# Performance work log

Hardware: AMD Instinct MI355X
Metric: run time of the kernel (lower is better)

## Reference

```python
import jax, jax.numpy as jnp
import numpy as np

LMAX = 2
NC = (LMAX + 1) ** 2          # 9 spherical-harmonic coefficients
C = 128                       # sphere/hidden channels (scalar_dim = 256//2)
CIN = 256                     # input/output irrep channels
EC = 16                       # edge channels (attn_weight_input_dim//2)
N_ATOM = 512
TOPK = 8
E = N_ATOM * TOPK
RES = 18                      # SO3 grid resolution

# m-primary permutation from CoefficientMapping(lmax=2, mmax=2).to_m:
# m=0 real [0,2,6]; m=1 real [3,7]; m=1 imag [1,5]; m=2 real [8]; m=2 imag [4]
PERM = np.array([0, 2, 6, 3, 7, 1, 5, 8, 4])
INV_PERM = np.argsort(PERM)
DEG = np.array([0, 1, 1, 1, 2, 2, 2, 2, 2])  # degree l of each coefficient


def _so2_block(em, x_edge, d0w, d0b, m0w1, m0w2,
               m1dw, m1db, m1w1r, m1w2r, m1w1i, m1w2i,
               m2dw, m2db, m2w1r, m2w2r, m2w1i, m2w2i):
    # em: [E, 9, C] (l-primary); x_edge: [E, EC]
    En = em.shape[0]
    em = em[:, PERM]                                  # -> m-primary order
    # m = 0 block (3 coefficients)
    g0 = jax.nn.silu(x_edge @ d0w + d0b)              # [E, C]
    x0 = em[:, 0:3].reshape(En, 3 * C)
    x0 = (((x0 @ m0w1) * g0) @ m0w2).reshape(En, 3, C)

    def so2_conv(xm, dw, db, w1r, w2r, w1i, w2i):
        # xm: [E, 2, k*C] with (real, imag) stacked on axis 1
        ge = jax.nn.silu(x_edge @ dw + db).reshape(En, 2, C)
        xr = jnp.einsum('eti,ih->eth', xm, w1r) * ge[:, 0:1]
        xr = jnp.einsum('eth,ho->eto', xr, w2r)
        xi = jnp.einsum('eti,ih->eth', xm, w1i) * ge[:, 1:2]
        xi = jnp.einsum('eth,ho->eto', xi, w2i)
        return jnp.stack([xr[:, 0] - xi[:, 1], xr[:, 1] + xi[:, 0]], axis=1)

    x1 = so2_conv(em[:, 3:7].reshape(En, 2, 2 * C), m1dw, m1db, m1w1r, m1w2r, m1w1i, m1w2i).reshape(En, 4, C)
    x2 = so2_conv(em[:, 7:9].reshape(En, 2, C), m2dw, m2db, m2w1r, m2w2r, m2w1i, m2w2i).reshape(En, 2, C)
    em = jnp.concatenate([x0, x1, x2], axis=1)
    return em[:, INV_PERM]                            # back to l-primary


def _forward(x, attn_weight, wigner, to_grid, from_grid, w_in, b_in, w_out, b_out,
             emb_src, emb_tgt, fc_dist_w, fc_dist_b, fc_edge_w, fc_edge_b,
             so2_dist0_w, so2_dist0_b, so2_m0_w1, so2_m0_w2,
             so2_m1_dist_w, so2_m1_dist_b, so2_m1_w1r, so2_m1_w2r, so2_m1_w1i, so2_m1_w2i,
             so2_m2_dist_w, so2_m2_dist_b, so2_m2_w1r, so2_m2_w2r, so2_m2_w1i, so2_m2_w2i,
             atomic_numbers, edge_src, attn_mask):
    N, topK = attn_weight.shape[:2]
    Eg = N * topK
    # proj_input: per-degree SO3 linear 256 -> 128, bias on l=0 only
    h = jnp.einsum('nic,ico->nio', x, w_in[DEG])
    h = h.at[:, 0, :].add(b_in)
    edge_tgt = jnp.repeat(jnp.arange(N), topK)
    # edge feature: dist MLP + source/target atom-type embedding gathers
    xe = attn_weight.reshape(Eg, -1) @ fc_dist_w + fc_dist_b
    xe = xe + emb_src[atomic_numbers][edge_src] + emb_tgt[atomic_numbers][edge_tgt]
    xe = jax.nn.silu(jax.nn.silu(xe) @ fc_edge_w + fc_edge_b)
    # gather node features to edges + rotate into edge frame (Wigner D)
    xs = jnp.einsum('eij,ejc->eic', wigner, h[edge_src])
    xt = jnp.einsum('eij,ejc->eic', wigner, h[edge_tgt])

    def blk(b, em):
        return _so2_block(em, xe, so2_dist0_w[b], so2_dist0_b[b], so2_m0_w1[b], so2_m0_w2[b],
                          so2_m1_dist_w[b], so2_m1_dist_b[b], so2_m1_w1r[b], so2_m1_w2r[b], so2_m1_w1i[b], so2_m1_w2i[b],
                          so2_m2_dist_w[b], so2_m2_dist_b[b], so2_m2_w1r[b], so2_m2_w2r[b], so2_m2_w1i[b], so2_m2_w2i[b])

    xt = blk(0, xs) + blk(1, xt)
    # grid activation: to-grid, SiLU, from-grid
    xg = jax.nn.silu(jnp.einsum('bai,eic->ebac', to_grid, xt))
    xt = jnp.einsum('bai,ebac->eic', from_grid, xg)
    # inverse rotation (orthogonal Wigner -> transpose)
    xt = jnp.einsum('eji,ejc->eic', wigner, xt)
    # mask invalid neighbors, scatter-sum over topK
    out = xt.reshape(N, topK, NC, C)
    out = jnp.where(attn_mask[:, :, None, None], 0.0, out).sum(axis=1)
    # proj_final: per-degree SO3 linear 128 -> 256
    out = jnp.einsum('nic,ico->nio', out, w_out[DEG])
    return out.at[:, 0, :].add(b_out)


def setup_inputs() -> dict:
    key = jax.random.key(0)
    ks = jax.random.split(key, 40)
    s = 0.05
    inp = {
        'x': jax.random.normal(ks[0], (N_ATOM, NC, CIN), jnp.float32),
        'attn_weight': jax.random.normal(ks[1], (N_ATOM, TOPK, 32), jnp.float32),
        'wigner': jax.random.normal(ks[2], (E, NC, NC), jnp.float32) * 0.3,
        'to_grid': jax.random.normal(ks[3], (RES, RES, NC), jnp.float32) * 0.2,
        'from_grid': jax.random.normal(ks[4], (RES, RES, NC), jnp.float32) * 0.2,
        'w_in': jax.random.normal(ks[5], (3, CIN, C), jnp.float32) * s,
        'b_in': jax.random.normal(ks[6], (C,), jnp.float32) * s,
        'w_out': jax.random.normal(ks[7], (3, C, CIN), jnp.float32) * s,
        'b_out': jax.random.normal(ks[8], (CIN,), jnp.float32) * s,
        'emb_src': jax.random.uniform(ks[9], (256, EC), jnp.float32, -0.001, 0.001),
        'emb_tgt': jax.random.uniform(ks[10], (256, EC), jnp.float32, -0.001, 0.001),
        'fc_dist_w': jax.random.normal(ks[11], (32, EC), jnp.float32) * s,
        'fc_dist_b': jax.random.normal(ks[12], (EC,), jnp.float32) * s,
        'fc_edge_w': jax.random.normal(ks[13], (EC, EC), jnp.float32) * s,
        'fc_edge_b': jax.random.normal(ks[14], (EC,), jnp.float32) * s,
        'so2_dist0_w': jax.random.normal(ks[15], (2, EC, C), jnp.float32) * s,
        'so2_dist0_b': jax.random.normal(ks[16], (2, C), jnp.float32) * s,
        'so2_m0_w1': jax.random.normal(ks[17], (2, 3 * C, C), jnp.float32) * s,
        'so2_m0_w2': jax.random.normal(ks[18], (2, C, 3 * C), jnp.float32) * s,
        'so2_m1_dist_w': jax.random.normal(ks[19], (2, EC, 2 * C), jnp.float32) * s,
        'so2_m1_dist_b': jax.random.normal(ks[20], (2, 2 * C), jnp.float32) * s,
        'so2_m1_w1r': jax.random.normal(ks[21], (2, 2 * C, C), jnp.float32) * s,
        'so2_m1_w2r': jax.random.normal(ks[22], (2, C, 2 * C), jnp.float32) * s,
        'so2_m1_w1i': jax.random.normal(ks[23], (2, 2 * C, C), jnp.float32) * s,
        'so2_m1_w2i': jax.random.normal(ks[24], (2, C, 2 * C), jnp.float32) * s,
        'so2_m2_dist_w': jax.random.normal(ks[25], (2, EC, 2 * C), jnp.float32) * s,
        'so2_m2_dist_b': jax.random.normal(ks[26], (2, 2 * C), jnp.float32) * s,
        'so2_m2_w1r': jax.random.normal(ks[27], (2, C, C), jnp.float32) * s,
        'so2_m2_w2r': jax.random.normal(ks[28], (2, C, C), jnp.float32) * s,
        'so2_m2_w1i': jax.random.normal(ks[29], (2, C, C), jnp.float32) * s,
        'so2_m2_w2i': jax.random.normal(ks[30], (2, C, C), jnp.float32) * s,
        'atomic_numbers': jax.random.randint(ks[31], (N_ATOM,), 0, 256),
        'edge_src': jax.random.randint(ks[32], (E,), 0, N_ATOM),
        'attn_mask': jax.random.randint(ks[33], (N_ATOM, TOPK), 0, 2).astype(bool),
    }
    return inp


def reference(x, attn_weight, wigner, to_grid, from_grid, w_in, b_in, w_out, b_out,
              emb_src, emb_tgt, fc_dist_w, fc_dist_b, fc_edge_w, fc_edge_b,
              so2_dist0_w, so2_dist0_b, so2_m0_w1, so2_m0_w2,
              so2_m1_dist_w, so2_m1_dist_b, so2_m1_w1r, so2_m1_w2r, so2_m1_w1i, so2_m1_w2i,
              so2_m2_dist_w, so2_m2_dist_b, so2_m2_w1r, so2_m2_w2r, so2_m2_w1i, so2_m2_w2i,
              atomic_numbers, edge_src, attn_mask):
    return _forward(x, attn_weight, wigner, to_grid, from_grid, w_in, b_in, w_out, b_out,
                    emb_src, emb_tgt, fc_dist_w, fc_dist_b, fc_edge_w, fc_edge_b,
                    so2_dist0_w, so2_dist0_b, so2_m0_w1, so2_m0_w2,
                    so2_m1_dist_w, so2_m1_dist_b, so2_m1_w1r, so2_m1_w2r, so2_m1_w1i, so2_m1_w2i,
                    so2_m2_dist_w, so2_m2_dist_b, so2_m2_w1r, so2_m2_w2r, so2_m2_w1i, so2_m2_w2i,
                    atomic_numbers, edge_src, attn_mask)
```

## Files before the change

### kernel.cpp

```cpp
#include <hip/hip_runtime.h>
#include <math.h>

typedef __attribute__((ext_vector_type(8))) short short8;
typedef __attribute__((ext_vector_type(4))) float f32x4;

__device__ const int d_PERM[9] = {0,2,6,3,7,1,5,8,4};
__device__ const int d_DEG[9]  = {0,1,1,1,2,2,2,2,2};

__device__ __forceinline__ float silu_f(float x){ return x / (1.0f + __expf(-x)); }

__device__ __forceinline__ unsigned short f2bf(float f){
  unsigned int u = __float_as_uint(f);
  return (unsigned short)((u + 0x7FFFu + ((u >> 16) & 1u)) >> 16);
}

__device__ __forceinline__ int mask_at(const void* mp, int flag, int e){
  if (flag==1) return ((const unsigned char*)mp)[e] != 0;
  if (flag==3) return ((const unsigned int*)mp)[2*e] != 0u;
  return ((const unsigned int*)mp)[e] != 0u;
}

__global__ void k_detect(const unsigned int* __restrict__ w, int* __restrict__ flag){
  __shared__ int notI, notF, anyOdd, anyEven;
  if (threadIdx.x==0){ notI=0; notF=0; anyOdd=0; anyEven=0; }
  __syncthreads();
  int li=0, lf=0, lo=0, le=0;
  for (int i = threadIdx.x; i < 1024; i += 256){
    unsigned int v = w[i];
    if (v != 0u && v != 1u) li = 1;
    if (v != 0u && v != 0x3F800000u) lf = 1;
    if (v != 0u){ if (i & 1) lo = 1; else le = 1; }
  }
  if (li) atomicOr(&notI,1);
  if (lf) atomicOr(&notF,1);
  if (lo) atomicOr(&anyOdd,1);
  if (le) atomicOr(&anyEven,1);
  __syncthreads();
  if (threadIdx.x==0){
    int f;
    if (!notI) f = (anyOdd || !anyEven) ? 0 : 3;
    else       f = (!notF) ? 2 : 1;
    *flag = f;
  }
}

__global__ __launch_bounds__(256) void k_compact(const void* __restrict__ maskp,
    const int* __restrict__ flagp, int* __restrict__ list, int* __restrict__ count){
  __shared__ int cnt[256];
  __shared__ int offs[256];
  int f = *flagp;
  int tid = threadIdx.x;
  int base = tid*16;
  int c = 0;
  for (int i=0;i<16;i++) if (!mask_at(maskp, f, base+i)) c++;
  cnt[tid] = c;
  __syncthreads();
  if (tid==0){
    int r = 0;
    for (int i=0;i<256;i++){ offs[i] = r; r += cnt[i]; }
    *count = r;
  }
  __syncthreads();
  int w = offs[tid];
  for (int i=0;i<16;i++){
    int e = base+i;
    if (!mask_at(maskp, f, e)) list[w++] = e;
  }
}

__global__ __launch_bounds__(128) void k_h(const float* __restrict__ x,
    const float* __restrict__ w_in, const float* __restrict__ b_in,
    float* __restrict__ H){
  __shared__ float xl[16][260];
  int i = blockIdx.y; int n0 = blockIdx.x*16;
  int deg = d_DEG[i];
  for (int idx = threadIdx.x; idx < 16*256; idx += 128){
    int r = idx >> 8, c = idx & 255;
    xl[r][c] = x[((size_t)(n0+r)*9 + i)*256 + c];
  }
  __syncthreads();
  int o = threadIdx.x;
  float acc[16];
  #pragma unroll
  for (int r=0;r<16;r++) acc[r]=0.f;
  const float* w = w_in + (size_t)deg*32768 + o;
  for (int c=0;c<256;c+=4){
    float w0=w[(size_t)c*128], w1=w[(size_t)(c+1)*128], w2=w[(size_t)(c+2)*128], w3=w[(size_t)(c+3)*128];
    #pragma unroll
    for (int r=0;r<16;r++){
      float4 xv4 = *(const float4*)&xl[r][c];
      acc[r] += xv4.x*w0 + xv4.y*w1 + xv4.z*w2 + xv4.w*w3;
    }
  }
  float bb = (i==0)? b_in[o] : 0.f;
  #pragma unroll
  for (int r=0;r<16;r++) H[((size_t)(n0+r)*9+i)*128+o] = acc[r]+bb;
}

__global__ __launch_bounds__(256) void k_xe(const float* __restrict__ attn,
    const float* __restrict__ fdw, const float* __restrict__ fdb,
    const float* __restrict__ few, const float* __restrict__ feb,
    const float* __restrict__ es, const float* __restrict__ et,
    const int* __restrict__ an, const int* __restrict__ esrc,
    float* __restrict__ XE){
  int e = blockIdx.x*256 + threadIdx.x;
  float aw[32];
  #pragma unroll
  for (int k=0;k<32;k+=4){
    float4 v = *(const float4*)&attn[(size_t)e*32+k];
    aw[k]=v.x; aw[k+1]=v.y; aw[k+2]=v.z; aw[k+3]=v.w;
  }
  int src = esrc[e]; int tgt = e>>3;
  int za = an[src], zb = an[tgt];
  float v0[16];
  #pragma unroll
  for (int j=0;j<16;j++){
    float s = fdb[j] + es[(size_t)za*16+j] + et[(size_t)zb*16+j];
    #pragma unroll
    for (int k=0;k<32;k++) s += aw[k]*fdw[k*16+j];
    v0[j] = silu_f(s);
  }
  #pragma unroll
  for (int j=0;j<16;j++){
    float s = feb[j];
    #pragma unroll
    for (int k=0;k<16;k++) s += v0[k]*few[k*16+j];
    XE[(size_t)e*16+j] = silu_f(s);
  }
}

__global__ __launch_bounds__(256) void k_wcvt(
    const float* __restrict__ m0w1, const float* __restrict__ m1w1r, const float* __restrict__ m1w1i,
    const float* __restrict__ m2w1r, const float* __restrict__ m2w1i,
    const float* __restrict__ m0w2, const float* __restrict__ m1w2r, const float* __restrict__ m1w2i,
    const float* __restrict__ m2w2r, const float* __restrict__ m2w2i,
    unsigned short* __restrict__ Wt)
{
  int base = (blockIdx.x*256 + threadIdx.x)*4;
  #pragma unroll
  for (int ii = 0; ii < 4; ii++){
    int idx = base + ii;
    float v;
    if (idx < 98304){
      int p = idx/49152, r = idx%49152, n = r/384, k = r%384;
      v = m0w1[p*49152 + k*128 + n];
    } else if (idx < 229376){
      int j = idx-98304; int q = j/32768, r = j%32768, n = r/256, k = r%256;
      const float* w = (q&1)?m1w1i:m1w1r;
      v = w[(q>>1)*32768 + k*128 + n];
    } else if (idx < 294912){
      int j = idx-229376; int q = j/16384, r = j%16384, n = r/128, k = r%128;
      const float* w = (q&1)?m2w1i:m2w1r;
      v = w[(q>>1)*16384 + k*128 + n];
    } else if (idx < 393216){
      int j = idx-294912; int n = j/256, k = j%256;
      v = m0w2[(k>>7)*49152 + (k&127)*384 + n];
    } else if (idx < 524288){
      int j = idx-393216; int n = j/512, k = j%512;
      const float* w = ((k>>7)&1)?m1w2i:m1w2r;
      v = w[(k>>8)*32768 + (k&127)*256 + n];
    } else {
      int j = idx-524288; int n = j/512, k = j%512;
      const float* w = ((k>>7)&1)?m2w2i:m2w2r;
      v = w[(k>>8)*16384 + (k&127)*128 + n];
    }
    Wt[idx] = f2bf(v);
  }
}

__global__ __launch_bounds__(256) void k_rotgate_m(
    const float* __restrict__ Hg, const float* __restrict__ XEg,
    const int* __restrict__ esrc, const float* __restrict__ wig,
    const float* __restrict__ d0w,  const float* __restrict__ d0b,
    const float* __restrict__ m1dw, const float* __restrict__ m1db,
    const float* __restrict__ m2dw, const float* __restrict__ m2db,
    unsigned short* __restrict__ XSb, unsigned short* __restrict__ XTb,
    float* __restrict__ G,
    const int* __restrict__ list, const int* __restrict__ countp, int s0)
{
  int slot = s0 + blockIdx.x;
  if (slot >= *countp) return;
  __shared__ float xe16[16];
  int e = list[slot];
  int el = blockIdx.x;
  int tid = threadIdx.x;
  int n = e >> 3, src = esrc[e];
  if (tid < 16) xe16[tid] = XEg[(size_t)e*16 + tid];
  for (int idx = tid; idx < 1152; idx += 256){
    int p = idx >> 7, c = idx & 127;
    int ch = d_PERM[p];
    const float* wr = wig + (size_t)e*81 + ch*9;
    const float* hs = Hg + (size_t)src*1152 + c;
    const float* ht = Hg + (size_t)n*1152 + c;
    float s1 = 0.f, s2 = 0.f;
    #pragma unroll
    for (int j = 0; j < 9; j++){
      float wv = wr[j];
      s1 += wv * hs[j*128];
      s2 += wv * ht[j*128];
    }
    XSb[(size_t)el*1152 + idx] = f2bf(s1);
    XTb[(size_t)el*1152 + idx] = f2bf(s2);
  }
  __syncthreads();
  for (int col = tid; col < 1280; col += 256){
    int b = col / 640, r = col % 640;
    const float* w; float bias; int ldw, c2;
    if (r < 128){       w = d0w  + (size_t)b*2048; c2 = r;     ldw = 128; bias = d0b[b*128 + c2]; }
    else if (r < 384){  w = m1dw + (size_t)b*4096; c2 = r-128; ldw = 256; bias = m1db[b*256 + c2]; }
    else {              w = m2dw + (size_t)b*4096; c2 = r-384; ldw = 256; bias = m2db[b*256 + c2]; }
    float s = bias;
    #pragma unroll
    for (int kk = 0; kk < 16; kk++) s += xe16[kk] * w[kk*ldw + c2];
    G[(size_t)el*1280 + col] = silu_f(s);
  }
}

__global__ __launch_bounds__(256) void k_gs1m(
    const unsigned short* __restrict__ XSb, const unsigned short* __restrict__ XTb,
    const float* __restrict__ G, const unsigned short* __restrict__ Wt,
    unsigned short* __restrict__ Pgb,
    const int* __restrict__ countp, int s0)
{
  int lc = *countp - s0;
  if (lc <= 0) return;
  if (lc > 2048) lc = 2048;
  int b = blockIdx.x, t = threadIdx.x;
  const unsigned short* Ax; const unsigned short* Bw;
  int K, bm, obase, goff, rsh, aoff, tstride;
  if (b < 64){
    int path = b & 1, mt = b >> 1;
    Ax = path ? XTb : XSb;
    Bw = Wt + path*49152;
    K = 384; bm = mt*64; obase = path*128; goff = path ? 640 : 0;
    rsh = 0; aoff = 0; tstride = 0;
  } else if (b < 320){
    int i = b-64; int q = i>>6, mt = i&63;
    Ax = (q>=2) ? XTb : XSb;
    Bw = Wt + 98304 + q*32768;
    K = 256; bm = mt*64; obase = 256 + q*256; goff = 128 + (q&1)*128 + (q>>1)*640;
    rsh = 1; aoff = 384; tstride = 256;
  } else {
    int i = b-320; int q = i>>6, mt = i&63;
    Ax = (q>=2) ? XTb : XSb;
    Bw = Wt + 229376 + q*16384;
    K = 128; bm = mt*64; obase = 1280 + q*256; goff = 384 + (q&1)*128 + (q>>1)*640;
    rsh = 1; aoff = 896; tstride = 128;
  }
  int rows = rsh ? 2*lc : lc;
  if (bm >= rows) return;
  int w = t >> 6, l = t & 63;
  int am = bm + w*16 + (l & 15);
  int ael = am >> rsh, atp = am & rsh;
  const unsigned short* aptr = Ax + (size_t)ael*1152 + aoff + atp*tstride + ((l>>4)*8);
  int bn = l & 15;
  int bko = (l>>4)*8;
  f32x4 acc[8];
  #pragma unroll
  for (int i=0;i<8;i++){ acc[i][0]=0.f; acc[i][1]=0.f; acc[i][2]=0.f; acc[i][3]=0.f; }
  for (int k0 = 0; k0 < K; k0 += 32){
    short8 a = *(const short8*)(aptr + k0);
    #pragma unroll
    for (int nt = 0; nt < 8; nt++){
      const unsigned short* bp = Bw + (size_t)(nt*16 + bn)*K + k0 + bko;
      short8 bb = *(const short8*)bp;
      acc[nt] = __builtin_amdgcn_mfma_f32_16x16x32_bf16(a, bb, acc[nt], 0, 0, 0);
    }
  }
  #pragma unroll
  for (int nt = 0; nt < 8; nt++){
    #pragma unroll
    for (int r = 0; r < 4; r++){
      int i2 = (l>>4)*4 + r;
      int m = bm + w*16 + i2;
      int el = m >> rsh, tp = m & rsh;
      int h = nt*16 + (l & 15);
      float v = acc[nt][r] * G[(size_t)el*1280 + goff + h];
      Pgb[(size_t)el*2304 + obase + tp*128 + h] = f2bf(v);
    }
  }
}

__global__ __launch_bounds__(256) void k_gs2m(
    const unsigned short* __restrict__ Pgb, const unsigned short* __restrict__ Wt2,
    float* __restrict__ Y,
    const int* __restrict__ countp, int s0)
{
  int lc = *countp - s0;
  if (lc <= 0) return;
  if (lc > 2048) lc = 2048;
  int b = blockIdx.x, t = threadIdx.x;
  int region, bm, ncb, K, rsh, segb;
  const unsigned short* Bw;
  if (b < 96){ region=0; int mt=b/3, nt3=b-mt*3; bm=mt*64; ncb=nt3*128; K=256; rsh=0; segb=0;    Bw = Wt2; }
  else if (b < 224){ region=1; int i=b-96; int mt=i>>1, nt2=i&1; bm=mt*64; ncb=nt2*128; K=512; rsh=1; segb=256;  Bw = Wt2 + 98304; }
  else { region=2; int mt=b-224; bm=mt*64; ncb=0; K=512; rsh=1; segb=1280; Bw = Wt2 + 229376; }
  int rows = rsh ? 2*lc : lc;
  if (bm >= rows) return;
  int w = t >> 6, l = t & 63;
  int am = bm + w*16 + (l & 15);
  int ael = am >> rsh, atp = am & rsh;
  int bko = (l>>4)*8;
  f32x4 acc[8];
  #pragma unroll
  for (int i=0;i<8;i++){ acc[i][0]=0.f; acc[i][1]=0.f; acc[i][2]=0.f; acc[i][3]=0.f; }
  for (int k0 = 0; k0 < K; k0 += 32){
    const unsigned short* ap;
    short sm = 0;
    if (region == 0){
      ap = Pgb + (size_t)ael*2304 + k0 + bko;
    } else {
      int seg = k0 >> 7, kk = k0 & 127;
      int tsel = (seg&1) ? (1-atp) : atp;
      sm = (short)(((seg&1) && atp==0) ? 0x8000 : 0);
      ap = Pgb + (size_t)ael*2304 + segb + seg*256 + tsel*128 + kk + bko;
    }
    short8 a = *(const short8*)ap;
    short8 smv = (short8)sm;
    a ^= smv;
    #pragma unroll
    for (int nt = 0; nt < 8; nt++){
      const unsigned short* bp = Bw + (size_t)(ncb + nt*16 + (l&15))*K + k0 + bko;
      short8 bb = *(const short8*)bp;
      acc[nt] = __builtin_amdgcn_mfma_f32_16x16x32_bf16(a, bb, acc[nt], 0, 0, 0);
    }
  }
  #pragma unroll
  for (int nt = 0; nt < 8; nt++){
    #pragma unroll
    for (int r = 0; r < 4; r++){
      int i2 = (l>>4)*4 + r;
      int m = bm + w*16 + i2;
      int el = m >> rsh, tp = m & rsh;
      int col = ncb + nt*16 + (l&15);
      int g = col >> 7, c = col & 127;
      int ch;
      if (region==0)      ch = (g==0) ? 0 : ((g==1) ? 2 : 6);
      else if (region==1) ch = tp ? (g ? 5 : 1) : (g ? 7 : 3);
      else                ch = tp ? 4 : 8;
      Y[(size_t)(s0 + el)*1152 + ch*128 + c] = acc[nt][r];
    }
  }
}

__global__ __launch_bounds__(256, 8) void k_grid9(const float* __restrict__ Y,
    const float* __restrict__ wig, const float* __restrict__ tg, const float* __restrict__ fg,
    const int* __restrict__ list, const int* __restrict__ countp,
    float* __restrict__ R)
{
  const int cnt = *countp;
  const int epair = blockIdx.x >> 1;
  const int half  = blockIdx.x & 1;
  const int base = epair*2;
  if (base >= cnt) return;
  __shared__ float cf[162*24];
  __shared__ float wl[2*81];
  int tid = threadIdx.x;
  int ok1 = (base+1 < cnt);
  int s2[2], e2[2];
  s2[0] = base;
  s2[1] = ok1 ? base+1 : base;
  e2[0] = list[s2[0]];
  e2[1] = list[s2[1]];

  const float* tgh = tg + half*1458;
  const float* fgh = fg + half*1458;
  for (int idx = tid; idx < 1458; idx += 256){
    int p = idx / 9, i = idx - p*9;
    cf[p*24 + i]      = tgh[idx];
    cf[p*24 + 12 + i] = fgh[idx];
  }
  for (int i = tid; i < 162; i += 256){
    int eL2 = i / 81, ii = i - eL2*81;
    wl[i] = wig[(size_t)e2[eL2]*81 + ii];
  }
  __syncthreads();

  int eL = tid >> 7, c = tid & 127;
  if (eL == 1 && !ok1) return;
  int slot = s2[eL], e = e2[eL];

  float y[9], z[9];
  #pragma unroll
  for (int i = 0; i < 9; i++){
    y[i] = Y[(size_t)slot*1152 + i*128 + c];
    z[i] = 0.f;
  }

  #pragma unroll 2
  for (int p = 0; p < 162; p++){
    const float* cp = &cf[p*24];
    float4 t0 = *(const float4*)cp;
    float4 t1 = *(const float4*)(cp+4);
    float  t8 = cp[8];
    float gp = t0.x*y[0] + t0.y*y[1] + t0.z*y[2] + t0.w*y[3]
             + t1.x*y[4] + t1.y*y[5] + t1.z*y[6] + t1.w*y[7] + t8*y[8];
    float s = gp * __fdividef(1.0f, 1.0f + __expf(-gp));
    float4 f0 = *(const float4*)(cp+12);
    float4 f1 = *(const float4*)(cp+16);
    float  f8 = cp[20];
    z[0] += f0.x*s; z[1] += f0.y*s; z[2] += f0.z*s; z[3] += f0.w*s;
    z[4] += f1.x*s; z[5] += f1.y*s; z[6] += f1.z*s; z[7] += f1.w*s; z[8] += f8*s;
  }

  const float* wle = &wl[eL*81];
  #pragma unroll
  for (int i2 = 0; i2 < 9; i2++){
    float s = 0.f;
    #pragma unroll
    for (int j = 0; j < 9; j++) s += wle[j*9 + i2] * z[j];
    atomicAdd(&R[(size_t)e*1152 + i2*128 + c], s);
  }
}

__global__ __launch_bounds__(256) void k_redout2(const float* __restrict__ R,
    const void* __restrict__ maskp, const int* __restrict__ flagp,
    const float* __restrict__ w_out, const float* __restrict__ b_out,
    float* __restrict__ out){
  __shared__ float sacc[128];
  int i2 = blockIdx.x; int n = blockIdx.y;
  int tid = threadIdx.x;
  int f = *flagp;
  if (tid < 128){
    float a = 0.f;
    for (int k = 0; k < 8; k++){
      int e = n*8 + k;
      if (!mask_at(maskp, f, e)) a += R[(size_t)e*1152 + i2*128 + tid];
    }
    sacc[tid] = a;
  }
  __syncthreads();
  int o = tid;
  int deg = d_DEG[i2];
  const float* wp = w_out + (size_t)deg*32768 + o;
  float s = (i2==0) ? b_out[o] : 0.f;
  #pragma unroll 4
  for (int c = 0; c < 128; c += 4){
    float4 a = *(const float4*)&sacc[c];
    s += a.x*wp[(size_t)c*256] + a.y*wp[(size_t)(c+1)*256]
       + a.z*wp[(size_t)(c+2)*256] + a.w*wp[(size_t)(c+3)*256];
  }
  out[((size_t)n*9 + i2)*256 + o] = s;
}

__device__ __forceinline__ float dotW(const float* __restrict__ A, const float* __restrict__ Wm, int K){
  float s = 0.f;
  #pragma unroll 4
  for (int i=0;i<K;i+=4){
    float4 a = *(const float4*)&A[i];
    s += a.x*Wm[(size_t)i*128] + a.y*Wm[(size_t)(i+1)*128]
       + a.z*Wm[(size_t)(i+2)*128] + a.w*Wm[(size_t)(i+3)*128];
  }
  return s;
}
__device__ __forceinline__ float dot2W(const float* __restrict__ P0, const float* __restrict__ P1,
    const float* __restrict__ W0, const float* __restrict__ W1, int ldw){
  float s = 0.f;
  #pragma unroll 4
  for (int k=0;k<128;k+=4){
    float4 a = *(const float4*)&P0[k];
    float4 b = *(const float4*)&P1[k];
    s += a.x*W0[(size_t)k*ldw] + a.y*W0[(size_t)(k+1)*ldw] + a.z*W0[(size_t)(k+2)*ldw] + a.w*W0[(size_t)(k+3)*ldw];
    s += b.x*W1[(size_t)k*ldw] + b.y*W1[(size_t)(k+1)*ldw] + b.z*W1[(size_t)(k+2)*ldw] + b.w*W1[(size_t)(k+3)*ldw];
  }
  return s;
}

__global__ __launch_bounds__(256) void k_mega(
    const float* __restrict__ x,      const float* __restrict__ w_in,  const float* __restrict__ b_in,
    const float* __restrict__ attn,
    const float* __restrict__ fdw,    const float* __restrict__ fdb,
    const float* __restrict__ few,    const float* __restrict__ feb,
    const float* __restrict__ es,     const float* __restrict__ et,
    const int*   __restrict__ an,     const int*   __restrict__ esrc,
    const float* __restrict__ d0w,    const float* __restrict__ d0b,
    const float* __restrict__ m1dw,   const float* __restrict__ m1db,
    const float* __restrict__ m2dw,   const float* __restrict__ m2db,
    const float* __restrict__ m0w1,   const float* __restrict__ m0w2,
    const float* __restrict__ m1w1r,  const float* __restrict__ m1w2r,
    const float* __restrict__ m1w1i,  const float* __restrict__ m1w2i,
    const float* __restrict__ m2w1r,  const float* __restrict__ m2w2r,
    const float* __restrict__ m2w1i,  const float* __restrict__ m2w2i,
    const float* __restrict__ wig,    const float* __restrict__ tg,   const float* __restrict__ fg,
    const float* __restrict__ w_out,  const float* __restrict__ b_out,
    const void*  __restrict__ maskp,  const int* __restrict__ flagp,
    float* __restrict__ out)
{
  __shared__ float S[7168];
  float* acc  = S;
  float* xs   = S + 1152;
  float* xtl  = S + 2304;
  float* Zb   = S + 1152;
  float* gg   = S + 3456;
  float* Yb   = S + 3456;
  float* P    = S + 4736;
  float* wl   = S + 7040;
  float* xe16 = S + 7124;
  float* xv   = S + 7140;

  const int n   = blockIdx.x;
  const int tid = threadIdx.x;
  const int f   = *flagp;

  for (int i = tid; i < 1152; i += 256) acc[i] = 0.f;

  for (int k = 0; k < 8; k++){
    int e = n*8 + k;
    if (mask_at(maskp, f, e)) continue;
    int src = esrc[e];
    __syncthreads();
    for (int i = tid; i < 81; i += 256) wl[i] = wig[(size_t)e*81 + i];
    if (tid < 16){
      int j = tid;
      float s = fdb[j] + es[(size_t)an[src]*16 + j] + et[(size_t)an[n]*16 + j];
      for (int kk = 0; kk < 32; kk++) s += attn[(size_t)e*32 + kk] * fdw[kk*16 + j];
      xv[j] = silu_f(s);
    }
    for (int idx = tid; idx < 2304; idx += 256){
      int which = idx >= 1152;
      int lidx = idx - which*1152;
      int j = lidx >> 7, c = lidx & 127;
      int deg = d_DEG[j];
      const float* wp = w_in + (size_t)deg*32768 + c;
      const float* xp = x + ((size_t)(which ? n : src)*9 + j)*256;
      float s = (j==0) ? b_in[c] : 0.f;
      for (int cc = 0; cc < 256; cc++) s += xp[cc] * wp[cc*128];
      P[idx] = s;
    }
    __syncthreads();
    if (tid < 16){
      int j = tid;
      float s = feb[j];
      for (int kk = 0; kk < 16; kk++) s += xv[kk] * few[kk*16 + j];
      xe16[j] = silu_f(s);
    }
    for (int idx = tid; idx < 1152; idx += 256){
      int p = idx >> 7, c = idx & 127;
      int ch = d_PERM[p];
      float s1 = 0.f, s2 = 0.f;
      #pragma unroll
      for (int j = 0; j < 9; j++){
        float wv = wl[ch*9 + j];
        s1 += wv * P[j*128 + c];
        s2 += wv * P[1152 + j*128 + c];
      }
      xs[idx]  = s1;
      xtl[idx] = s2;
    }
    __syncthreads();
    for (int col = tid; col < 1280; col += 256){
      int b = col / 640, r = col % 640;
      const float* w; float bias; int ldw, c2;
      if (r < 128){       w = d0w  + (size_t)b*2048; c2 = r;     ldw = 128; bias = d0b[b*128 + c2]; }
      else if (r < 384){  w = m1dw + (size_t)b*4096; c2 = r-128; ldw = 256; bias = m1db[b*256 + c2]; }
      else {              w = m2dw + (size_t)b*4096; c2 = r-384; ldw = 256; bias = m2db[b*256 + c2]; }
      float s = bias;
      #pragma unroll
      for (int kk = 0; kk < 16; kk++) s += xe16[kk] * w[kk*ldw + c2];
      gg[col] = silu_f(s);
    }
    __syncthreads();
    for (int o = tid; o < 2304; o += 256){
      float s;
      if (o < 256){
        int path = o >> 7, h = o & 127;
        s = dotW(path ? xtl : xs, m0w1 + (size_t)path*49152 + h, 384);
      } else if (o < 1280){
        int q = (o-256) >> 8; int rem = (o-256) & 255; int t = rem >> 7, h = rem & 127;
        const float* A  = ((q>=2) ? xtl : xs) + 384 + t*256;
        const float* Wm = ((q&1) ? m1w1i : m1w1r) + (size_t)((q>=2)?1:0)*32768 + h;
        s = dotW(A, Wm, 256);
      } else {
        int q = (o-1280) >> 8; int rem = (o-1280) & 255; int t = rem >> 7, h = rem & 127;
        const float* A  = ((q>=2) ? xtl : xs) + 896 + t*128;
        const float* Wm = ((q&1) ? m2w1i : m2w1r) + (size_t)((q>=2)?1:0)*16384 + h;
        s = dotW(A, Wm, 128);
      }
      P[o] = s;
    }
    __syncthreads();
    for (int o = tid; o < 2304; o += 256){
      int h = o & 127, goff;
      if (o < 256) goff = (o >> 7) ? 640 : 0;
      else if (o < 1280){ int q = (o-256) >> 8;  goff = 128 + (q&1)*128 + (q>>1)*640; }
      else              { int q = (o-1280) >> 8; goff = 384 + (q&1)*128 + (q>>1)*640; }
      P[o] *= gg[goff + h];
    }
    __syncthreads();
    for (int o = tid; o < 1152; o += 256){
      float s; int ch, c;
      if (o < 384){
        int g = o >> 7; c = o & 127;
        ch = (g==0) ? 0 : ((g==1) ? 2 : 6);
        const float* w0 = m0w2 + o;
        s = dot2W(P, P+128, w0, w0+49152, 384);
      } else if (o < 896){
        int om = o - 384; int tp = om >> 8; int col = om & 255;
        int g = col >> 7; c = col & 127;
        ch = tp ? (g ? 5 : 1) : (g ? 7 : 3);
        float sgn = tp ? 1.f : -1.f;
        const float* wr = m1w2r + col;
        const float* wi = m1w2i + col;
        s = dot2W(P+256+tp*128,     P+768+tp*128,     wr, wr+32768, 256)
          + sgn * dot2W(P+512+(1-tp)*128, P+1024+(1-tp)*128, wi, wi+32768, 256);
      } else {
        int om = o - 896; int tp = om >> 7; c = om & 127;
        ch = tp ? 4 : 8;
        float sgn = tp ? 1.f : -1.f;
        const float* wr = m2w2r + c;
        const float* wi = m2w2i + c;
        s = dot2W(P+1280+tp*128,     P+1792+tp*128,     wr, wr+16384, 128)
          + sgn * dot2W(P+1536+(1-tp)*128, P+2048+(1-tp)*128, wi, wi+16384, 128);
      }
      Yb[ch*128 + c] = s;
    }
    __syncthreads();
    {
      int half = tid >> 7, c = tid & 127;
      float z[9];
      #pragma unroll
      for (int i = 0; i < 9; i++) z[i] = 0.f;
      float y[9];
      #pragma unroll
      for (int i = 0; i < 9; i++) y[i] = Yb[i*128 + c];
      int p0 = half*162, p1 = p0 + 162;
      #pragma unroll 2
      for (int p = p0; p < p1; p++){
        float gp = 0.f;
        #pragma unroll
        for (int i = 0; i < 9; i++) gp += tg[p*9 + i] * y[i];
        float s = silu_f(gp);
        #pragma unroll
        for (int i = 0; i < 9; i++) z[i] += fg[p*9 + i] * s;
      }
      #pragma unroll
      for (int i = 0; i < 9; i++) Zb[half*1152 + i*128 + c] = z[i];
    }
    __syncthreads();
    for (int idx = tid; idx < 1152; idx += 256){
      int i2 = idx >> 7, c = idx & 127;
      float s = 0.f;
      #pragma unroll
      for (int j = 0; j < 9; j++)
        s += wl[j*9 + i2] * (Zb[j*128 + c] + Zb[1152 + j*128 + c]);
      acc[idx] += s;
    }
  }
  __syncthreads();
  {
    int o = tid;
    for (int i2 = 0; i2 < 9; i2++){
      int deg = d_DEG[i2];
      const float* wp = w_out + (size_t)deg*32768 + o;
      float s = (i2==0) ? b_out[o] : 0.f;
      #pragma unroll 4
      for (int c = 0; c < 128; c += 4){
        float4 a = *(const float4*)&acc[i2*128 + c];
        s += a.x*wp[(size_t)c*256] + a.y*wp[(size_t)(c+1)*256]
           + a.z*wp[(size_t)(c+2)*256] + a.w*wp[(size_t)(c+3)*256];
      }
      out[((size_t)n*9 + i2)*256 + o] = s;
    }
  }
}

extern "C" void kernel_launch(void* const* d_in, const int* in_sizes, int n_in,
                              void* d_out, int out_size, void* d_ws, size_t ws_size,
                              hipStream_t stream){
  const float* x     = (const float*)d_in[0];
  const float* attn  = (const float*)d_in[1];
  const float* wig   = (const float*)d_in[2];
  const float* tg    = (const float*)d_in[3];
  const float* fg    = (const float*)d_in[4];
  const float* w_in  = (const float*)d_in[5];
  const float* b_in  = (const float*)d_in[6];
  const float* w_out = (const float*)d_in[7];
  const float* b_out = (const float*)d_in[8];
  const float* es    = (const float*)d_in[9];
  const float* et    = (const float*)d_in[10];
  const float* fdw   = (const float*)d_in[11];
  const float* fdb   = (const float*)d_in[12];
  const float* few   = (const float*)d_in[13];
  const float* feb   = (const float*)d_in[14];
  const float* d0w   = (const float*)d_in[15];
  const float* d0b   = (const float*)d_in[16];
  const float* m0w1  = (const float*)d_in[17];
  const float* m0w2  = (const float*)d_in[18];
  const float* m1dw  = (const float*)d_in[19];
  const float* m1db  = (const float*)d_in[20];
  const float* m1w1r = (const float*)d_in[21];
  const float* m1w2r = (const float*)d_in[22];
  const float* m1w1i = (const float*)d_in[23];
  const float* m1w2i = (const float*)d_in[24];
  const float* m2dw  = (const float*)d_in[25];
  const float* m2db  = (const float*)d_in[26];
  const float* m2w1r = (const float*)d_in[27];
  const float* m2w2r = (const float*)d_in[28];
  const float* m2w1i = (const float*)d_in[29];
  const float* m2w2i = (const float*)d_in[30];
  const int*   an    = (const int*)d_in[31];
  const int*   esrc  = (const int*)d_in[32];
  const void*  maskp = d_in[33];

  int*   ip  = (int*)d_ws;
  int* FLAG  = ip + 0;
  int* COUNT = ip + 1;
  int* LIST  = ip + 16;
  float* W   = (float*)d_ws;
  float* Hg1  = W + 4112;
  float* XEg1 = Hg1 + 589824;
  float* XS1  = XEg1 + 65536;
  float* XT1  = XS1 + 2359296;
  float* Gg1  = XT1 + 2359296;
  float* Pg1  = Gg1 + 2621440;
  float* Yf   = Pg1 + 4718592;
  float* Rf   = XS1;
  unsigned short* XSb = (unsigned short*)XS1;
  unsigned short* XTb = XSb + 2359296;
  unsigned short* Pgb = XSb + 4718592;
  unsigned short* Wtb = (unsigned short*)Pg1;
  size_t need_t1 = (size_t)(4112 + 589824 + 65536 + 2359296 + 2359296 + 2621440 + 4718592 + 4718592) * 4;

  k_detect<<<1,256,0,stream>>>((const unsigned int*)maskp, FLAG);

  if (ws_size >= need_t1){
    k_compact<<<1,256,0,stream>>>(maskp, FLAG, LIST, COUNT);
    k_h<<<dim3(32,9),128,0,stream>>>(x, w_in, b_in, Hg1);
    k_xe<<<16,256,0,stream>>>(attn, fdw, fdb, few, feb, es, et, an, esrc, XEg1);
    k_wcvt<<<576,256,0,stream>>>(m0w1, m1w1r, m1w1i, m2w1r, m2w1i,
                                 m0w2, m1w2r, m1w2i, m2w2r, m2w2i, Wtb);
    for (int c2 = 0; c2 < 2; c2++){
      int s0 = c2*2048;
      k_rotgate_m<<<2048,256,0,stream>>>(Hg1, XEg1, esrc, wig,
          d0w, d0b, m1dw, m1db, m2dw, m2db, XSb, XTb, Gg1, LIST, COUNT, s0);
      k_gs1m<<<576,256,0,stream>>>(XSb, XTb, Gg1, Wtb, Pgb, COUNT, s0);
      k_gs2m<<<288,256,0,stream>>>(Pgb, Wtb + 294912, Yf, COUNT, s0);
    }
    hipMemsetAsync(Rf, 0, (size_t)4718592*4, stream);
    k_grid9<<<4096,256,0,stream>>>(Yf, wig, tg, fg, LIST, COUNT, Rf);
    k_redout2<<<dim3(9,512),256,0,stream>>>(Rf, maskp, FLAG, w_out, b_out, (float*)d_out);
  } else {
    k_mega<<<512,256,0,stream>>>(
        x, w_in, b_in, attn, fdw, fdb, few, feb, es, et, an, esrc,
        d0w, d0b, m1dw, m1db, m2dw, m2db,
        m0w1, m0w2, m1w1r, m1w2r, m1w1i, m1w2i, m2w1r, m2w2r, m2w1i, m2w2i,
        wig, tg, fg, w_out, b_out, maskp, FLAG, (float*)d_out);
  }
}
```

Measured before the change: 315.4 us.

## Compute SO3 grid projection with bf16 MFMA and drop atomic accumulation

Replaces the scalar FP32 grid kernel with an MFMA-based one. It projects coefficients to grid points, applies SiLU, and projects back with 16x16x32 bf16 matrix instructions, using a one-time repacked bf16 copy of the to/from grid matrices. The previous GEMM now writes its output as bf16 in a channel-major padded layout suited to the MFMA operand. Each edge's result is written directly instead of through atomicAdd, which also removes the float memset of R. The cost is bf16 rounding of the activations and grid values, plus a new memset of the padded Y buffer.

```diff
diff --git a/kernel.cpp b/kernel.cpp
--- a/kernel.cpp
+++ b/kernel.cpp
@@ -2,6 +2,7 @@
 #include <math.h>
 
 typedef __attribute__((ext_vector_type(8))) short short8;
+typedef __attribute__((ext_vector_type(4))) short short4_t;
 typedef __attribute__((ext_vector_type(4))) float f32x4;
 
 __device__ const int d_PERM[9] = {0,2,6,3,7,1,5,8,4};
@@ -165,6 +166,26 @@
       v = w[(k>>8)*16384 + (k&127)*128 + n];
     }
     Wt[idx] = f2bf(v);
+  }
+}
+
+__global__ __launch_bounds__(256) void k_fprep(const float* __restrict__ tg,
+    const float* __restrict__ fg,
+    unsigned short* __restrict__ tgA, unsigned short* __restrict__ fgA)
+{
+  for (int idx = threadIdx.x; idx < 11264; idx += 256){
+    int pt = idx >> 9, rem = idx & 511, l = rem >> 3, j = rem & 7;
+    int p = pt*16 + (l & 15);
+    int i = (l >> 4)*8 + j;
+    float v = (p < 324 && i < 9) ? tg[p*9 + i] : 0.f;
+    tgA[idx] = f2bf(v);
+  }
+  for (int idx = threadIdx.x; idx < 5632; idx += 256){
+    int sb = idx >> 9, rem = idx & 511, l = rem >> 3, j = rem & 7;
+    int p = sb*32 + (l >> 4)*8 + j;
+    int i = l & 15;
+    float v = (p < 324 && i < 9) ? fg[p*9 + i] : 0.f;
+    fgA[idx] = f2bf(v);
   }
 }
 
@@ -283,7 +304,7 @@
 
 __global__ __launch_bounds__(256) void k_gs2m(
     const unsigned short* __restrict__ Pgb, const unsigned short* __restrict__ Wt2,
-    float* __restrict__ Y,
+    unsigned short* __restrict__ Ybt,
     const int* __restrict__ countp, int s0)
 {
   int lc = *countp - s0;
@@ -338,78 +359,71 @@
       if (region==0)      ch = (g==0) ? 0 : ((g==1) ? 2 : 6);
       else if (region==1) ch = tp ? (g ? 5 : 1) : (g ? 7 : 3);
       else                ch = tp ? 4 : 8;
-      Y[(size_t)(s0 + el)*1152 + ch*128 + c] = acc[nt][r];
-    }
-  }
-}
-
-__global__ __launch_bounds__(256, 8) void k_grid9(const float* __restrict__ Y,
-    const float* __restrict__ wig, const float* __restrict__ tg, const float* __restrict__ fg,
+      Ybt[(size_t)(s0 + el)*2048 + c*16 + ch] = f2bf(acc[nt][r]);
+    }
+  }
+}
+
+__global__ __launch_bounds__(256) void k_gridm(
+    const unsigned short* __restrict__ Ybt,
+    const unsigned short* __restrict__ tgA, const unsigned short* __restrict__ fgA,
+    const float* __restrict__ wig,
     const int* __restrict__ list, const int* __restrict__ countp,
     float* __restrict__ R)
 {
-  const int cnt = *countp;
-  const int epair = blockIdx.x >> 1;
-  const int half  = blockIdx.x & 1;
-  const int base = epair*2;
-  if (base >= cnt) return;
-  __shared__ float cf[162*24];
-  __shared__ float wl[2*81];
+  int slot = blockIdx.x;
+  if (slot >= *countp) return;
+  __shared__ float wl[81];
+  __shared__ unsigned short Sld[4][512];
+  __shared__ float Zld[4][256];
   int tid = threadIdx.x;
-  int ok1 = (base+1 < cnt);
-  int s2[2], e2[2];
-  s2[0] = base;
-  s2[1] = ok1 ? base+1 : base;
-  e2[0] = list[s2[0]];
-  e2[1] = list[s2[1]];
-
-  const float* tgh = tg + half*1458;
-  const float* fgh = fg + half*1458;
-  for (int idx = tid; idx < 1458; idx += 256){
-    int p = idx / 9, i = idx - p*9;
-    cf[p*24 + i]      = tgh[idx];
-    cf[p*24 + 12 + i] = fgh[idx];
-  }
-  for (int i = tid; i < 162; i += 256){
-    int eL2 = i / 81, ii = i - eL2*81;
-    wl[i] = wig[(size_t)e2[eL2]*81 + ii];
-  }
-  __syncthreads();
-
-  int eL = tid >> 7, c = tid & 127;
-  if (eL == 1 && !ok1) return;
-  int slot = s2[eL], e = e2[eL];
-
-  float y[9], z[9];
-  #pragma unroll
-  for (int i = 0; i < 9; i++){
-    y[i] = Y[(size_t)slot*1152 + i*128 + c];
-    z[i] = 0.f;
-  }
-
-  #pragma unroll 2
-  for (int p = 0; p < 162; p++){
-    const float* cp = &cf[p*24];
-    float4 t0 = *(const float4*)cp;
-    float4 t1 = *(const float4*)(cp+4);
-    float  t8 = cp[8];
-    float gp = t0.x*y[0] + t0.y*y[1] + t0.z*y[2] + t0.w*y[3]
-             + t1.x*y[4] + t1.y*y[5] + t1.z*y[6] + t1.w*y[7] + t8*y[8];
-    float s = gp * __fdividef(1.0f, 1.0f + __expf(-gp));
-    float4 f0 = *(const float4*)(cp+12);
-    float4 f1 = *(const float4*)(cp+16);
-    float  f8 = cp[20];
-    z[0] += f0.x*s; z[1] += f0.y*s; z[2] += f0.z*s; z[3] += f0.w*s;
-    z[4] += f1.x*s; z[5] += f1.y*s; z[6] += f1.z*s; z[7] += f1.w*s; z[8] += f8*s;
-  }
-
-  const float* wle = &wl[eL*81];
-  #pragma unroll
-  for (int i2 = 0; i2 < 9; i2++){
-    float s = 0.f;
-    #pragma unroll
-    for (int j = 0; j < 9; j++) s += wle[j*9 + i2] * z[j];
-    atomicAdd(&R[(size_t)e*1152 + i2*128 + c], s);
+  int e = list[slot];
+  for (int i = tid; i < 81; i += 256) wl[i] = wig[(size_t)e*81 + i];
+  __syncthreads();
+  int w = tid >> 6, l = tid & 63;
+  int lcn = l & 15, lg = l >> 4;
+  const unsigned short* ybase = Ybt + (size_t)slot*2048;
+
+  for (int ct = 0; ct < 2; ct++){
+    int c0 = (w*2 + ct)*16;
+    short8 bfA = (short8)(short)0;
+    if (lg < 2) bfA = *(const short8*)(ybase + (c0 + lcn)*16 + lg*8);
+    f32x4 Z; Z[0]=0.f; Z[1]=0.f; Z[2]=0.f; Z[3]=0.f;
+    for (int sb = 0; sb < 11; sb++){
+      f32x4 s0; s0[0]=0.f; s0[1]=0.f; s0[2]=0.f; s0[3]=0.f;
+      f32x4 s1 = s0;
+      short8 a0 = *(const short8*)(tgA + (size_t)(sb*2+0)*512 + l*8);
+      short8 a1 = *(const short8*)(tgA + (size_t)(sb*2+1)*512 + l*8);
+      s0 = __builtin_amdgcn_mfma_f32_16x16x32_bf16(a0, bfA, s0, 0, 0, 0);
+      s1 = __builtin_amdgcn_mfma_f32_16x16x32_bf16(a1, bfA, s1, 0, 0, 0);
+      short4_t pk0, pk1;
+      #pragma unroll
+      for (int r = 0; r < 4; r++){
+        float v0 = s0[r]; v0 = v0 * __fdividef(1.0f, 1.0f + __expf(-v0));
+        float v1 = s1[r]; v1 = v1 * __fdividef(1.0f, 1.0f + __expf(-v1));
+        pk0[r] = (short)f2bf(v0);
+        pk1[r] = (short)f2bf(v1);
+      }
+      *(short4_t*)&Sld[w][lcn*32 + lg*4]      = pk0;
+      *(short4_t*)&Sld[w][lcn*32 + 16 + lg*4] = pk1;
+      short8 af = *(const short8*)(fgA + (size_t)sb*512 + l*8);
+      short8 bs = *(const short8*)&Sld[w][lcn*32 + lg*8];
+      Z = __builtin_amdgcn_mfma_f32_16x16x32_bf16(af, bs, Z, 0, 0, 0);
+    }
+    *(f32x4*)&Zld[w][lcn*16 + lg*4] = Z;
+    float zc[9];
+    #pragma unroll
+    for (int j = 0; j < 9; j++) zc[j] = Zld[w][lcn*16 + j];
+    #pragma unroll
+    for (int t2 = 0; t2 < 3; t2++){
+      int i2 = lg + t2*4;
+      if (i2 < 9){
+        float r = 0.f;
+        #pragma unroll
+        for (int j = 0; j < 9; j++) r += wl[j*9 + i2] * zc[j];
+        R[(size_t)e*1152 + i2*128 + c0 + lcn] = r;
+      }
+    }
   }
 }
 
@@ -719,6 +733,9 @@
   unsigned short* XTb = XSb + 2359296;
   unsigned short* Pgb = XSb + 4718592;
   unsigned short* Wtb = (unsigned short*)Pg1;
+  unsigned short* tgAb = Wtb + 655360;
+  unsigned short* fgAb = tgAb + 11264;
+  unsigned short* Ybt  = (unsigned short*)Yf;
   size_t need_t1 = (size_t)(4112 + 589824 + 65536 + 2359296 + 2359296 + 2621440 + 4718592 + 4718592) * 4;
 
   k_detect<<<1,256,0,stream>>>((const unsigned int*)maskp, FLAG);
@@ -729,15 +746,16 @@
     k_xe<<<16,256,0,stream>>>(attn, fdw, fdb, few, feb, es, et, an, esrc, XEg1);
     k_wcvt<<<576,256,0,stream>>>(m0w1, m1w1r, m1w1i, m2w1r, m2w1i,
                                  m0w2, m1w2r, m1w2i, m2w2r, m2w2i, Wtb);
+    k_fprep<<<1,256,0,stream>>>(tg, fg, tgAb, fgAb);
+    hipMemsetAsync(Ybt, 0, (size_t)8388608*2, stream);
     for (int c2 = 0; c2 < 2; c2++){
       int s0 = c2*2048;
       k_rotgate_m<<<2048,256,0,stream>>>(Hg1, XEg1, esrc, wig,
           d0w, d0b, m1dw, m1db, m2dw, m2db, XSb, XTb, Gg1, LIST, COUNT, s0);
       k_gs1m<<<576,256,0,stream>>>(XSb, XTb, Gg1, Wtb, Pgb, COUNT, s0);
-      k_gs2m<<<288,256,0,stream>>>(Pgb, Wtb + 294912, Yf, COUNT, s0);
-    }
-    hipMemsetAsync(Rf, 0, (size_t)4718592*4, stream);
-    k_grid9<<<4096,256,0,stream>>>(Yf, wig, tg, fg, LIST, COUNT, Rf);
+      k_gs2m<<<288,256,0,stream>>>(Pgb, Wtb + 294912, Ybt, COUNT, s0);
+    }
+    k_gridm<<<4096,256,0,stream>>>(Ybt, tgAb, fgAb, wig, LIST, COUNT, Rf);
     k_redout2<<<dim3(9,512),256,0,stream>>>(Rf, maskp, FLAG, w_out, b_out, (float*)d_out);
   } else {
     k_mega<<<512,256,0,stream>>>(
```

New measurement: 305.6 us. 1.03x faster.
